# Performance work log

Hardware: AMD Instinct MI355X
Metric: run time of the kernel (lower is better)

Reference implementation:

```python
import jax, jax.numpy as jnp
import numpy as np
import math

N_HEAD = 16
D_MODEL = 1024
D_HEAD = 64
GRID = 28


def _alibi_slopes(heads):
    def pow2(n):
        start = 2 ** (-(2 ** (-(math.log2(n) - 3))))
        return [start * (start ** i) for i in range(n)]
    if math.log2(heads).is_integer():
        return pow2(heads)
    c = 2 ** math.floor(math.log2(heads))
    return pow2(c) + pow2(2 * c)[0::2][: heads - c]


def _teeth_bias(heads):
    # bias[i,j] = |i%14 - j%14| + |i//14 - j//14| (loop in get_bias overwrites the -|j-i| init)
    idx = np.arange(GRID)
    row, col = idx // 14, idx % 14
    b = np.abs(col[:, None] - col[None, :]) + np.abs(row[:, None] - row[None, :])  # [28,28]
    slopes = np.asarray(_alibi_slopes(heads), dtype=np.float32)  # [h]
    return jnp.asarray(slopes[:, None, None] * b[None].astype(np.float32))  # [h,28,28]


def _layer_norm(x, gamma, beta, eps=1e-5):
    mu = jnp.mean(x, axis=-1, keepdims=True)
    var = jnp.var(x, axis=-1, keepdims=True)
    return (x - mu) * jax.lax.rsqrt(var + eps) * gamma + beta


def setup_inputs() -> dict:
    key = jax.random.key(0)
    ks = jax.random.split(key, 6)
    s = 0.02
    return {
        "hidden": jax.random.normal(ks[0], (2048, GRID, D_MODEL), dtype=jnp.float32),
        "wq": jax.random.normal(ks[1], (D_MODEL, N_HEAD * D_HEAD), dtype=jnp.float32) * s,
        "wk": jax.random.normal(ks[2], (D_MODEL, N_HEAD * D_HEAD), dtype=jnp.float32) * s,
        "wv": jax.random.normal(ks[3], (D_MODEL, N_HEAD * D_HEAD), dtype=jnp.float32) * s,
        "wo": jax.random.normal(ks[4], (N_HEAD * D_HEAD, D_MODEL), dtype=jnp.float32) * s,
        "gamma": jnp.ones((D_MODEL,), dtype=jnp.float32),
        "beta": jnp.zeros((D_MODEL,), dtype=jnp.float32),
    }


def reference(hidden, wq, wk, wv, wo, gamma, beta):
    b, s, _ = hidden.shape
    # pre_lnorm: hidden is reassigned to LN(hidden); combined == hidden (memory=None)
    h = _layer_norm(hidden, gamma, beta)
    q = (h @ wq).reshape(b, s, N_HEAD, D_HEAD).transpose(0, 2, 1, 3)  # [b,h,s,d]
    k = (h @ wk).reshape(b, s, N_HEAD, D_HEAD).transpose(0, 2, 1, 3)
    v = (h @ wv).reshape(b, s, N_HEAD, D_HEAD).transpose(0, 2, 1, 3)
    # NOTE: original forward never applies atten_scale -> unscaled dots (faithful)
    scores = jnp.einsum("bhid,bhjd->bhij", q, k)
    scores = scores + _teeth_bias(N_HEAD)[None, :, :s, :s]
    attn = jax.nn.softmax(scores, axis=-1)
    ctx = jnp.einsum("bhij,bhjd->bhid", attn, v)
    ctx = ctx.transpose(0, 2, 1, 3).reshape(b, s, N_HEAD * D_HEAD)
    out = ctx @ wo
    return h + out  # pre_lnorm residual uses the normalized hidden
```

## Files before the change

### kernel.cpp

```cpp
#include <hip/hip_runtime.h>
#include <hip/hip_bf16.h>

typedef unsigned short u16;
typedef __attribute__((ext_vector_type(8))) short bf16x8;
typedef __attribute__((ext_vector_type(4))) float f32x4;

#define DEVINL __device__ __forceinline__

DEVINL u16 f2b(float f) {
    __hip_bfloat16 h = __float2bfloat16(f);
    return __builtin_bit_cast(u16, h);
}
DEVINL float b2f(u16 u) {
    unsigned int x = ((unsigned int)u) << 16;
    return __builtin_bit_cast(float, x);
}
DEVINL int iabs(int x) { return x < 0 ? -x : x; }
DEVINL f32x4 MFMA(bf16x8 a, bf16x8 b, f32x4 c) {
    return __builtin_amdgcn_mfma_f32_16x16x32_bf16(a, b, c, 0, 0, 0);
}

#define GL2LDS(g, s)                                                                     \
    __builtin_amdgcn_global_load_lds(                                                    \
        (const __attribute__((address_space(1))) unsigned int*)(g),                      \
        (__attribute__((address_space(3))) unsigned int*)(s), 16, 0, 0)

__global__ __launch_bounds__(256) void wconv_kernel(const float* __restrict__ wq,
                                                    const float* __restrict__ wk,
                                                    const float* __restrict__ wv,
                                                    const float* __restrict__ wo,
                                                    u16* __restrict__ wqkvt,
                                                    u16* __restrict__ wot) {
    __shared__ float tile[32][33];
    int z = blockIdx.z;
    const float* src = (z == 0) ? wq : (z == 1) ? wk : (z == 2) ? wv : wo;
    int n0 = blockIdx.x * 32, k0 = blockIdx.y * 32;
    int r0 = threadIdx.x >> 5, c = threadIdx.x & 31;
#pragma unroll
    for (int i = 0; i < 4; i++) {
        int r = r0 + i * 8;
        tile[r][c] = src[(size_t)(k0 + r) * 1024 + n0 + c];
    }
    __syncthreads();
    u16* dst = (z < 3) ? wqkvt : wot;
#pragma unroll
    for (int i = 0; i < 4; i++) {
        int r = r0 + i * 8;
        int nn = n0 + r;
        size_t drow = (z < 3) ? ((size_t)(nn >> 6) * 192 + (size_t)z * 64 + (nn & 63))
                              : (size_t)nn;
        dst[drow * 1024 + k0 + c] = f2b(tile[c][r]);
    }
}

__global__ __launch_bounds__(256) void ln_kernel(const float* __restrict__ x,
                                                 const float* __restrict__ gamma,
                                                 const float* __restrict__ beta,
                                                 u16* __restrict__ h) {
    int w = threadIdx.x >> 6, l = threadIdx.x & 63;
    size_t row = (size_t)blockIdx.x * 4 + w;
    const float4* xr = (const float4*)(x + row * 1024);
    float4 v[4];
    float s = 0.f, sq = 0.f;
#pragma unroll
    for (int i = 0; i < 4; i++) {
        v[i] = xr[l + i * 64];
        s += v[i].x + v[i].y + v[i].z + v[i].w;
        sq += v[i].x * v[i].x + v[i].y * v[i].y + v[i].z * v[i].z + v[i].w * v[i].w;
    }
#pragma unroll
    for (int off = 1; off < 64; off <<= 1) {
        s += __shfl_xor(s, off);
        sq += __shfl_xor(sq, off);
    }
    float mu = s * (1.f / 1024.f);
    float var = sq * (1.f / 1024.f) - mu * mu;
    float rstd = rsqrtf(var + 1e-5f);
    const float4* g4 = (const float4*)gamma;
    const float4* b4 = (const float4*)beta;
#pragma unroll
    for (int i = 0; i < 4; i++) {
        float4 g = g4[l + i * 64], b = b4[l + i * 64];
        float y0 = (v[i].x - mu) * rstd * g.x + b.x;
        float y1 = (v[i].y - mu) * rstd * g.y + b.y;
        float y2 = (v[i].z - mu) * rstd * g.z + b.z;
        float y3 = (v[i].w - mu) * rstd * g.w + b.w;
        unsigned int lo = (unsigned int)f2b(y0) | ((unsigned int)f2b(y1) << 16);
        unsigned int hi = (unsigned int)f2b(y2) | ((unsigned int)f2b(y3) << 16);
        uint2 pk;
        pk.x = lo;
        pk.y = hi;
        *(uint2*)(h + row * 1024 + (size_t)(l + i * 64) * 4) = pk;
    }
}

__global__ __launch_bounds__(256, 3) void fused_qkv_attn(const u16* __restrict__ h,
                                                         const u16* __restrict__ wqkvt,
                                                         u16* __restrict__ ctx) {
    __shared__ __align__(16) char smem[50944];
    char* sA = smem;
    char* sB = smem + 16384;
    int t = threadIdx.x;

    int nwg = gridDim.x;
    int cpx = nwg >> 3;
    int wg = ((int)blockIdx.x & 7) * cpx + ((int)blockIdx.x >> 3);
    int x = wg >> 10;
    int i0 = wg & 1023;
    int bm = i0 >> 1;
    int head = (x << 1) | (i0 & 1);

    int p16 = t * 16;
    int srow = p16 >> 7;
    int scolb = (p16 & 127) ^ ((srow & 7) << 4);
    const char* aB = (const char*)h + ((size_t)bm * 112 + srow) * 2048 + scolb;
    const char* bB = (const char*)wqkvt + ((size_t)head * 192 + srow) * 2048 + scolb;

    int l = t & 63, w = t >> 6, g = l >> 4, lr = l & 15;
    int swz = (lr & 7) << 4;

    f32x4 acc[7][3];
#pragma unroll
    for (int m = 0; m < 7; m++)
#pragma unroll
        for (int n = 0; n < 3; n++) acc[m][n] = {0.f, 0.f, 0.f, 0.f};

#pragma unroll 1
    for (int kt = 0; kt < 16; ++kt) {
        int kb = kt * 128;
#pragma unroll
        for (int i = 0; i < 4; i++) GL2LDS(aB + (size_t)i * 65536 + kb, sA + i * 4096 + p16);
#pragma unroll
        for (int i = 0; i < 6; i++) GL2LDS(bB + (size_t)i * 65536 + kb, sB + i * 4096 + p16);
        __syncthreads();
#pragma unroll
        for (int ks = 0; ks < 2; ++ks) {
            bf16x8 af[7], bfv[3];
#pragma unroll
            for (int m = 0; m < 7; m++)
                af[m] = *(const bf16x8*)(sA + (m * 16 + lr) * 128 + ((ks * 64 + g * 16) ^ swz));
#pragma unroll
            for (int n = 0; n < 3; n++)
                bfv[n] = *(const bf16x8*)(sB + (w * 48 + n * 16 + lr) * 128 +
                                          ((ks * 64 + g * 16) ^ swz));
#pragma unroll
            for (int m = 0; m < 7; m++)
#pragma unroll
                for (int n = 0; n < 3; n++) acc[m][n] = MFMA(af[m], bfv[n], acc[m][n]);
        }
        __syncthreads();
    }

    u16(*qkb)[136] = (u16(*)[136])smem;
    u16(*vt)[64][40] = (u16(*)[64][40])(smem + 30464);

    {
        int s2 = t >> 6, d = t & 63;
#pragma unroll
        for (int j = 28; j < 32; ++j) vt[s2][d][j] = 0;
    }
#pragma unroll
    for (int m = 0; m < 7; m++)
#pragma unroll
        for (int n = 0; n < 3; n++) {
            int col = w * 48 + n * 16 + lr;
#pragma unroll
            for (int r = 0; r < 4; ++r) {
                int row = m * 16 + g * 4 + r;
                u16 val = f2b(acc[m][n][r]);
                if (col < 128) {
                    qkb[row][col] = val;
                } else {
                    int d = col - 128;
                    int s2 = row / 28;
                    int j = row - s2 * 28;
                    vt[s2][d][j] = val;
                }
            }
        }
    __syncthreads();

    int rbase = w * 28;
    f32x4 sc[2][2];
#pragma unroll
    for (int a = 0; a < 2; a++)
#pragma unroll
        for (int c = 0; c < 2; c++) sc[a][c] = {0.f, 0.f, 0.f, 0.f};
#pragma unroll
    for (int c = 0; c < 2; c++) {
        int off = c * 64 + g * 16;
        const char* r0p = (const char*)&qkb[rbase + lr][0];
        const char* r1p = (const char*)&qkb[rbase + 16 + lr][0];
        bf16x8 a0 = *(const bf16x8*)(r0p + off);
        bf16x8 a1 = *(const bf16x8*)(r1p + off);
        bf16x8 b0 = *(const bf16x8*)(r0p + 128 + off);
        bf16x8 b1 = *(const bf16x8*)(r1p + 128 + off);
        sc[0][0] = MFMA(a0, b0, sc[0][0]);
        sc[0][1] = MFMA(a0, b1, sc[0][1]);
        sc[1][0] = MFMA(a1, b0, sc[1][0]);
        sc[1][1] = MFMA(a1, b1, sc[1][1]);
    }

    u16(*sp)[40] = (u16(*)[40])((char*)smem + w * 7616);

    float slope = exp2f(-0.5f * (float)(head + 1));
    int j0 = lr, j1 = 16 + lr;
    int j0m = j0 % 14, j0d = j0 / 14;
    int j1m = j1 % 14, j1d = j1 / 14;
#pragma unroll
    for (int it = 0; it < 2; ++it) {
#pragma unroll
        for (int r = 0; r < 4; ++r) {
            int i = it * 16 + g * 4 + r;
            int im = i % 14, id = i / 14;
            float s0 = sc[it][0][r] + slope * (float)(iabs(im - j0m) + iabs(id - j0d));
            float s1 = (j1 < 28)
                           ? sc[it][1][r] + slope * (float)(iabs(im - j1m) + iabs(id - j1d))
                           : -1e30f;
            float mx = fmaxf(s0, s1);
#pragma unroll
            for (int off = 1; off < 16; off <<= 1) mx = fmaxf(mx, __shfl_xor(mx, off));
            float e0 = __expf(s0 - mx), e1 = __expf(s1 - mx);
            float sm = e0 + e1;
#pragma unroll
            for (int off = 1; off < 16; off <<= 1) sm += __shfl_xor(sm, off);
            float inv = 1.f / sm;
            sp[i][lr] = f2b(e0 * inv);
            sp[i][16 + lr] = f2b(e1 * inv);
        }
    }

    bf16x8 pa0 = *(const bf16x8*)&sp[lr][g * 8];
    bf16x8 pa1 = *(const bf16x8*)&sp[16 + lr][g * 8];
    f32x4 o[2][4];
#pragma unroll
    for (int a = 0; a < 2; a++)
#pragma unroll
        for (int d = 0; d < 4; d++) o[a][d] = {0.f, 0.f, 0.f, 0.f};
#pragma unroll
    for (int dt = 0; dt < 4; ++dt) {
        bf16x8 bv = *(const bf16x8*)&vt[w][dt * 16 + lr][g * 8];
        o[0][dt] = MFMA(pa0, bv, o[0][dt]);
        o[1][dt] = MFMA(pa1, bv, o[1][dt]);
    }
#pragma unroll
    for (int it = 0; it < 2; ++it)
#pragma unroll
        for (int dt = 0; dt < 4; ++dt)
#pragma unroll
            for (int r = 0; r < 4; ++r) {
                int i = it * 16 + g * 4 + r;
                if (i < 28) {
                    size_t off =
                        ((size_t)(bm * 4 + w) * 28 + i) * 1024 + head * 64 + dt * 16 + lr;
                    ctx[off] = f2b(o[it][dt][r]);
                }
            }
}

template <int OUT_BF16, int RESID>
__global__ __launch_bounds__(256, 2) void gemm_bt(const u16* __restrict__ A,
                                                  const u16* __restrict__ Bt,
                                                  void* __restrict__ Cv,
                                                  const u16* __restrict__ resid,
                                                  int lda, int ldc) {
    __shared__ u16 smem[16384];
    int t = threadIdx.x;

    int nwg = gridDim.x;
    int cpx = nwg >> 3;
    int wg = (blockIdx.x & 7) * cpx + (blockIdx.x >> 3);
    const int sgrp = 448 * 8;
    int sn = wg / sgrp;
    int rem = wg - sn * sgrp;
    int bm = rem >> 3;
    int bn = sn * 8 + (rem & 7);

    const char* Ab = (const char*)A;
    const char* Bb = (const char*)Bt;
    size_t aoffg[4], boffg[4];
#pragma unroll
    for (int i = 0; i < 4; i++) {
        int p = t * 16 + i * 4096;
        int row = p >> 7;
        int colb = (p & 127) ^ ((row & 7) << 4);
        aoffg[i] = (size_t)(bm * 128 + row) * (size_t)lda * 2 + colb;
        boffg[i] = (size_t)(bn * 128 + row) * 2048 + colb;
    }
    char* sA = (char*)smem;
    char* sB = sA + 16384;

    int l = t & 63, w = t >> 6;
    int wm = w >> 1, wn = w & 1, g = l >> 4, lr = l & 15;
    int swz = (lr & 7) << 4;

    f32x4 acc[4][4];
#pragma unroll
    for (int m = 0; m < 4; m++)
#pragma unroll
        for (int n = 0; n < 4; n++) acc[m][n] = {0.f, 0.f, 0.f, 0.f};

    for (int kt = 0; kt < 16; ++kt) {
        int kb = kt * 128;
#pragma unroll
        for (int i = 0; i < 4; i++) GL2LDS(Ab + aoffg[i] + kb, sA + i * 4096 + t * 16);
#pragma unroll
        for (int i = 0; i < 4; i++) GL2LDS(Bb + boffg[i] + kb, sB + i * 4096 + t * 16);
        __syncthreads();
#pragma unroll
        for (int ks = 0; ks < 2; ++ks) {
            bf16x8 af[4], bfv[4];
#pragma unroll
            for (int m = 0; m < 4; m++)
                af[m] = *(const bf16x8*)(sA + (wm * 64 + m * 16 + lr) * 128 +
                                         ((ks * 64 + g * 16) ^ swz));
#pragma unroll
            for (int n = 0; n < 4; n++)
                bfv[n] = *(const bf16x8*)(sB + (wn * 64 + n * 16 + lr) * 128 +
                                          ((ks * 64 + g * 16) ^ swz));
#pragma unroll
            for (int m = 0; m < 4; m++)
#pragma unroll
                for (int n = 0; n < 4; n++)
                    acc[m][n] = MFMA(af[m], bfv[n], acc[m][n]);
        }
        __syncthreads();
    }

    size_t row0 = (size_t)bm * 128 + wm * 64;
    int col0 = bn * 128 + wn * 64;
    if (OUT_BF16) {
        u16* C = (u16*)Cv;
#pragma unroll
        for (int m = 0; m < 4; m++)
#pragma unroll
            for (int n = 0; n < 4; n++)
#pragma unroll
                for (int r = 0; r < 4; r++) {
                    size_t rr = row0 + m * 16 + g * 4 + r;
                    int cc = col0 + n * 16 + lr;
                    C[rr * (size_t)ldc + cc] = f2b(acc[m][n][r]);
                }
    } else {
        float* C = (float*)Cv;
#pragma unroll
        for (int m = 0; m < 4; m++)
#pragma unroll
            for (int n = 0; n < 4; n++)
#pragma unroll
                for (int r = 0; r < 4; r++) {
                    size_t rr = row0 + m * 16 + g * 4 + r;
                    int cc = col0 + n * 16 + lr;
                    float o = acc[m][n][r];
                    if (RESID) o += b2f(resid[rr * 1024 + cc]);
                    C[rr * (size_t)ldc + cc] = o;
                }
    }
}

extern "C" void kernel_launch(void* const* d_in, const int* in_sizes, int n_in,
                              void* d_out, int out_size, void* d_ws, size_t ws_size,
                              hipStream_t stream) {
    (void)in_sizes; (void)n_in; (void)out_size; (void)ws_size;
    const float* hidden = (const float*)d_in[0];
    const float* wq = (const float*)d_in[1];
    const float* wk = (const float*)d_in[2];
    const float* wv = (const float*)d_in[3];
    const float* wo = (const float*)d_in[4];
    const float* gamma = (const float*)d_in[5];
    const float* beta = (const float*)d_in[6];
    float* out = (float*)d_out;

    char* ws = (char*)d_ws;
    u16* h = (u16*)ws;
    u16* ctx = (u16*)(ws + 117440512);
    u16* wqkvt = (u16*)(ws + 234881024);
    u16* wot = (u16*)(ws + 234881024 + 6291456);

    wconv_kernel<<<dim3(32, 32, 4), 256, 0, stream>>>(wq, wk, wv, wo, wqkvt, wot);
    ln_kernel<<<14336, 256, 0, stream>>>(hidden, gamma, beta, h);
    fused_qkv_attn<<<8192, 256, 0, stream>>>(h, wqkvt, ctx);
    gemm_bt<0, 1><<<448 * 8, 256, 0, stream>>>(ctx, wot, out, h, 1024, 1024);
}
```

Before: 647.0 us.

## Shrink LDS footprint to fit four workgroups per CU in fused QKV-attention

Cuts the shared memory of the fused QKV+attention kernel so four workgroups can be resident per CU instead of three, and raises launch_bounds to match. It loads only the 112 valid A rows, writes Q/K with an XOR-swizzled unpadded layout, and gives the softmax probabilities their own region. V is written into the reused Q/K area only after softmax, which adds an extra barrier phase. The higher occupancy target may force register spilling, since the accumulator arrays are large.

```diff
diff --git a/kernel.cpp b/kernel.cpp
--- a/kernel.cpp
+++ b/kernel.cpp
@@ -94,12 +94,12 @@
     }
 }
 
-__global__ __launch_bounds__(256, 3) void fused_qkv_attn(const u16* __restrict__ h,
+__global__ __launch_bounds__(256, 4) void fused_qkv_attn(const u16* __restrict__ h,
                                                          const u16* __restrict__ wqkvt,
                                                          u16* __restrict__ ctx) {
-    __shared__ __align__(16) char smem[50944];
+    __shared__ __align__(16) char smem[38912];
     char* sA = smem;
-    char* sB = smem + 16384;
+    char* sB = smem + 14336;
     int t = threadIdx.x;
 
     int nwg = gridDim.x;
@@ -129,7 +129,8 @@
     for (int kt = 0; kt < 16; ++kt) {
         int kb = kt * 128;
 #pragma unroll
-        for (int i = 0; i < 4; i++) GL2LDS(aB + (size_t)i * 65536 + kb, sA + i * 4096 + p16);
+        for (int i = 0; i < 3; i++) GL2LDS(aB + (size_t)i * 65536 + kb, sA + i * 4096 + p16);
+        if (t < 128) GL2LDS(aB + (size_t)3 * 65536 + kb, sA + 3 * 4096 + p16);
 #pragma unroll
         for (int i = 0; i < 6; i++) GL2LDS(bB + (size_t)i * 65536 + kb, sB + i * 4096 + p16);
         __syncthreads();
@@ -151,30 +152,20 @@
         __syncthreads();
     }
 
-    u16(*qkb)[136] = (u16(*)[136])smem;
-    u16(*vt)[64][40] = (u16(*)[64][40])(smem + 30464);
-
-    {
-        int s2 = t >> 6, d = t & 63;
-#pragma unroll
-        for (int j = 28; j < 32; ++j) vt[s2][d][j] = 0;
-    }
+    u16* qkb = (u16*)smem;
+    u16(*sp)[40] = (u16(*)[40])(smem + 28672 + w * 2560);
+    u16(*vt)[64][40] = (u16(*)[64][40])smem;
+
 #pragma unroll
     for (int m = 0; m < 7; m++)
 #pragma unroll
         for (int n = 0; n < 3; n++) {
             int col = w * 48 + n * 16 + lr;
-#pragma unroll
-            for (int r = 0; r < 4; ++r) {
-                int row = m * 16 + g * 4 + r;
-                u16 val = f2b(acc[m][n][r]);
-                if (col < 128) {
-                    qkb[row][col] = val;
-                } else {
-                    int d = col - 128;
-                    int s2 = row / 28;
-                    int j = row - s2 * 28;
-                    vt[s2][d][j] = val;
+            if (col < 128) {
+#pragma unroll
+                for (int r = 0; r < 4; ++r) {
+                    int row = m * 16 + g * 4 + r;
+                    qkb[row * 128 + (col ^ ((row & 7) << 3))] = f2b(acc[m][n][r]);
                 }
             }
         }
@@ -188,20 +179,17 @@
         for (int c = 0; c < 2; c++) sc[a][c] = {0.f, 0.f, 0.f, 0.f};
 #pragma unroll
     for (int c = 0; c < 2; c++) {
-        int off = c * 64 + g * 16;
-        const char* r0p = (const char*)&qkb[rbase + lr][0];
-        const char* r1p = (const char*)&qkb[rbase + 16 + lr][0];
-        bf16x8 a0 = *(const bf16x8*)(r0p + off);
-        bf16x8 a1 = *(const bf16x8*)(r1p + off);
-        bf16x8 b0 = *(const bf16x8*)(r0p + 128 + off);
-        bf16x8 b1 = *(const bf16x8*)(r1p + 128 + off);
+        int r0 = rbase + lr, r1 = rbase + 16 + lr;
+        int u0 = c * 32 + g * 8;
+        bf16x8 a0 = *(const bf16x8*)&qkb[r0 * 128 + (u0 ^ ((r0 & 7) << 3))];
+        bf16x8 a1 = *(const bf16x8*)&qkb[r1 * 128 + (u0 ^ ((r1 & 7) << 3))];
+        bf16x8 b0 = *(const bf16x8*)&qkb[r0 * 128 + ((64 + u0) ^ ((r0 & 7) << 3))];
+        bf16x8 b1 = *(const bf16x8*)&qkb[r1 * 128 + ((64 + u0) ^ ((r1 & 7) << 3))];
         sc[0][0] = MFMA(a0, b0, sc[0][0]);
         sc[0][1] = MFMA(a0, b1, sc[0][1]);
         sc[1][0] = MFMA(a1, b0, sc[1][0]);
         sc[1][1] = MFMA(a1, b1, sc[1][1]);
     }
-
-    u16(*sp)[40] = (u16(*)[40])((char*)smem + w * 7616);
 
     float slope = exp2f(-0.5f * (float)(head + 1));
     int j0 = lr, j1 = 16 + lr;
@@ -229,6 +217,30 @@
             sp[i][16 + lr] = f2b(e1 * inv);
         }
     }
+    __syncthreads();
+
+    {
+        int s2 = t >> 6, d = t & 63;
+#pragma unroll
+        for (int j = 28; j < 32; ++j) vt[s2][d][j] = 0;
+    }
+#pragma unroll
+    for (int m = 0; m < 7; m++)
+#pragma unroll
+        for (int n = 0; n < 3; n++) {
+            int col = w * 48 + n * 16 + lr;
+            if (col >= 128) {
+#pragma unroll
+                for (int r = 0; r < 4; ++r) {
+                    int row = m * 16 + g * 4 + r;
+                    int d = col - 128;
+                    int s2 = row / 28;
+                    int j = row - s2 * 28;
+                    vt[s2][d][j] = f2b(acc[m][n][r]);
+                }
+            }
+        }
+    __syncthreads();
 
     bf16x8 pa0 = *(const bf16x8*)&sp[lr][g * 8];
     bf16x8 pa1 = *(const bf16x8*)&sp[16 + lr][g * 8];
```

New measurement: 626.9 us (median of 2 runs). -3.1%, faster.
